# Optimization experiments

Measured on AMD Instinct MI355X. Metric: run time of the kernel, lower is better.

The kernel has to match this reference:

```python
import jax, jax.numpy as jnp
import numpy as np

B, G, D, H, DH, M, L, FF = 4, 16906, 256, 8, 32, 110, 6, 1024
EPS = 1e-4  # performer_pytorch softmax_kernel eps

def _ortho_proj(rng, m, d):
    # gaussian orthogonal random matrix (FAVOR+), rows scaled by chi norms
    blocks = []
    for _ in range(m // d):
        q, _ = np.linalg.qr(rng.standard_normal((d, d)))
        blocks.append(q.T)
    rem = m % d
    if rem:
        q, _ = np.linalg.qr(rng.standard_normal((d, d)))
        blocks.append(q.T[:rem])
    mat = np.concatenate(blocks, 0)
    mult = np.linalg.norm(rng.standard_normal((m, d)), axis=1)
    return (mult[:, None] * mat).astype(np.float32)

def setup_inputs():
    key = jax.random.key(0)
    ks = jax.random.split(key, 12)
    rng = np.random.default_rng(0)
    s = 0.02
    return {
        'expr': jax.random.uniform(ks[0], (B, G), jnp.float32),
        'token_emb': jax.random.normal(ks[1], (7, D)) * s,
        'cls_token': jax.random.normal(ks[2], (1, 1, D)),
        'ln1_g': jnp.ones((L, D)), 'ln1_b': jnp.zeros((L, D)),
        'wq': jax.random.normal(ks[3], (L, D, D)) * s, 'bq': jnp.zeros((L, D)),
        'wk': jax.random.normal(ks[4], (L, D, D)) * s, 'bk': jnp.zeros((L, D)),
        'wv': jax.random.normal(ks[5], (L, D, D)) * s, 'bv': jnp.zeros((L, D)),
        'wo': jax.random.normal(ks[6], (L, D, D)) * s, 'bo': jnp.zeros((L, D)),
        'ln2_g': jnp.ones((L, D)), 'ln2_b': jnp.zeros((L, D)),
        'w1': jax.random.normal(ks[7], (L, D, FF)) * s, 'b1': jnp.zeros((L, FF)),
        'w2': jax.random.normal(ks[8], (L, FF, D)) * s, 'b2': jnp.zeros((L, D)),
        'proj_w': jax.random.normal(ks[9], (D, D)) * s, 'proj_b': jnp.zeros((D,)),
        'projs': jnp.asarray(np.stack([_ortho_proj(rng, M, DH) for _ in range(L)])),
    }

def _ln(x, g, b):
    mu = jnp.mean(x, -1, keepdims=True)
    var = jnp.mean((x - mu) ** 2, -1, keepdims=True)
    return (x - mu) * jax.lax.rsqrt(var + 1e-5) * g + b

def _feat(x, proj, is_query):
    # FAVOR+ softmax kernel feature map. x: [b,h,n,dh], proj: [m,dh]
    xn = x * (DH ** -0.25)
    dd = jnp.einsum('bhnd,md->bhnm', xn, proj)
    diag = 0.5 * jnp.sum(xn * xn, -1, keepdims=True)
    stab = jnp.max(dd, -1, keepdims=True) if is_query else jnp.max(dd)
    return (M ** -0.5) * (jnp.exp(dd - diag - stab) + EPS)

def _heads(x, w, bias, b, n):
    return (x @ w + bias).reshape(b, n, H, DH).transpose(0, 2, 1, 3)

def _forward(expr, token_emb, cls_token, ln1_g, ln1_b, wq, bq, wk, bk, wv, bv,
             wo, bo, ln2_g, ln2_b, w1, b1, w2, b2, proj_w, proj_b, projs):
    b = expr.shape[0]
    # preprocess: L1-normalize, scale, log1p, 7-bin bucketize
    sexpr = expr / jnp.maximum(jnp.sum(jnp.abs(expr), -1, keepdims=True), 1e-12)
    e = jnp.log1p(sexpr * 1e4)
    bins = jnp.linspace(0.0, jnp.max(e), 8)[:7]
    tokens = jnp.clip(jnp.searchsorted(bins, e, side='left'), 0, 6)
    x = jnp.concatenate([jnp.broadcast_to(cls_token, (b, 1, D)), token_emb[tokens]], 1)
    n = x.shape[1]
    for l in range(L):
        h = _ln(x, ln1_g[l], ln1_b[l])
        q = _heads(h, wq[l], bq[l], b, n)
        k = _heads(h, wk[l], bk[l], b, n)
        v = _heads(h, wv[l], bv[l], b, n)
        qf = _feat(q, projs[l], True)
        kf = _feat(k, projs[l], False)
        # non-causal linear attention: phi(Q)(phi(K)^T V) / (phi(Q) sum phi(K))
        d_inv = 1.0 / jnp.einsum('bhnm,bhm->bhn', qf, jnp.sum(kf, 2))
        ctx = jnp.einsum('bhnm,bhnd->bhmd', kf, v)
        o = jnp.einsum('bhnm,bhmd,bhn->bhnd', qf, ctx, d_inv)
        x = x + o.transpose(0, 2, 1, 3).reshape(b, n, D) @ wo[l] + bo[l]
        h = _ln(x, ln2_g[l], ln2_b[l])
        x = x + jax.nn.gelu(h @ w1[l] + b1[l], approximate=False) @ w2[l] + b2[l]
    return x[:, 0] @ proj_w + proj_b

def reference(expr, token_emb, cls_token, ln1_g, ln1_b, wq, bq, wk, bk, wv, bv,
              wo, bo, ln2_g, ln2_b, w1, b1, w2, b2, proj_w, proj_b, projs):
    return _forward(expr, token_emb, cls_token, ln1_g, ln1_b, wq, bq, wk, bk, wv,
                    bv, wo, bo, ln2_g, ln2_b, w1, b1, w2, b2, proj_w, proj_b, projs)
```

## Files before the change

kernel.cpp:

```cpp
#include <hip/hip_runtime.h>
#include <math.h>

#define B_ 4
#define G_ 16906
#define D_ 256
#define H_ 8
#define DH_ 32
#define M_ 110
#define L_ 6
#define FF_ 1024
#define NSEQ (G_ + 1)
#define NR (B_ * NSEQ)
#define NRP_ 67712
#define NYT_ 529
#define BH_ 32
#define QS_ 768

static constexpr float SCALE_  = 0.42044820762685725f;
static constexpr float MSCALE_ = 0.09534625892455922f;
static constexpr float FEPS_   = 1e-4f;

#define SZP_ ((size_t)NRP_ * D_)
#define WS_FLOATS 92000000
__device__ float g_ws[WS_FLOATS];

typedef __attribute__((ext_vector_type(8))) short bh8;
typedef __attribute__((ext_vector_type(4))) float f4;

__device__ __forceinline__ unsigned f2u(float f){
    unsigned u = __float_as_uint(f);
    return (u & 0x80000000u) ? ~u : (u | 0x80000000u);
}
__device__ __forceinline__ float u2f(unsigned u){
    return (u & 0x80000000u) ? __uint_as_float(u & 0x7fffffffu) : __uint_as_float(~u);
}
__device__ __forceinline__ unsigned short f2b(float f){
    unsigned u = __float_as_uint(f);
    return (unsigned short)((u + 0x7fffu + ((u >> 16) & 1u)) >> 16);
}
__device__ __forceinline__ float bf2f(unsigned short u){
    return __uint_as_float(((unsigned)u) << 16);
}
__device__ __forceinline__ void gld16(const unsigned short* g, unsigned short* l){
    __builtin_amdgcn_global_load_lds((const __attribute__((address_space(1))) void*)g,
                                     (__attribute__((address_space(3))) void*)l, 16, 0, 0);
}

__global__ void k_pre_init(unsigned* __restrict__ maxkey){
    if (threadIdx.x == 0) *maxkey = 0x007fffffu;
}

__global__ void k_rowsum(const float* __restrict__ expr, float* __restrict__ ssum){
    int b = blockIdx.x, t = threadIdx.x;
    float s = 0.f;
    for (int g = t; g < G_; g += 256) s += fabsf(expr[(size_t)b * G_ + g]);
    __shared__ float red[256];
    red[t] = s; __syncthreads();
    for (int off = 128; off > 0; off >>= 1){ if (t < off) red[t] += red[t + off]; __syncthreads(); }
    if (t == 0) ssum[b] = red[0];
}

__global__ void k_compute_e(const float* __restrict__ expr, const float* __restrict__ ssum,
                            float* __restrict__ ebuf, unsigned* __restrict__ maxkey){
    int t = threadIdx.x;
    int idx = blockIdx.x * 256 + t;
    float e = -INFINITY;
    if (idx < B_ * G_){
        int b = idx / G_;
        float denom = fmaxf(ssum[b], 1e-12f);
        e = log1pf(expr[idx] / denom * 1e4f);
        ebuf[idx] = e;
    }
    __shared__ float red[256];
    red[t] = e; __syncthreads();
    for (int off = 128; off > 0; off >>= 1){ if (t < off) red[t] = fmaxf(red[t], red[t + off]); __syncthreads(); }
    if (t == 0) atomicMax(maxkey, f2u(red[0]));
}

__global__ void k_embed(const float* __restrict__ ebuf, const unsigned* __restrict__ maxkey,
                        const float* __restrict__ tokemb, const float* __restrict__ cls,
                        float* __restrict__ x){
    int row = blockIdx.x, t = threadIdx.x;
    if (row >= NR){ x[(size_t)row * D_ + t] = 0.f; return; }
    int b = row / NSEQ, i = row % NSEQ;
    float v;
    if (i == 0){
        v = cls[t];
    } else {
        float e = ebuf[(size_t)b * G_ + (i - 1)];
        float mx = u2f(*maxkey);
        float step = mx / 7.0f;
        int cnt = 0;
        #pragma unroll
        for (int j = 0; j < 7; ++j){
            float bin = step * (float)j;
            cnt += (bin < e) ? 1 : 0;
        }
        if (cnt > 6) cnt = 6;
        v = tokemb[cnt * D_ + t];
    }
    x[(size_t)row * D_ + t] = v;
}

__launch_bounds__(256)
__global__ void k_ln(const float* __restrict__ X, unsigned short* __restrict__ Y,
                     const float* __restrict__ g, const float* __restrict__ b){
    int wave = threadIdx.x >> 6, lane = threadIdx.x & 63;
    int row = blockIdx.x * 4 + wave;
    float4 v = *(const float4*)&X[(size_t)row * D_ + lane * 4];
    float s = v.x + v.y + v.z + v.w;
    s += __shfl_xor(s, 1);  s += __shfl_xor(s, 2);  s += __shfl_xor(s, 4);
    s += __shfl_xor(s, 8);  s += __shfl_xor(s, 16); s += __shfl_xor(s, 32);
    float mu = s * (1.0f / 256.0f);
    float d0 = v.x - mu, d1 = v.y - mu, d2 = v.z - mu, d3 = v.w - mu;
    float q = d0 * d0 + d1 * d1 + d2 * d2 + d3 * d3;
    q += __shfl_xor(q, 1);  q += __shfl_xor(q, 2);  q += __shfl_xor(q, 4);
    q += __shfl_xor(q, 8);  q += __shfl_xor(q, 16); q += __shfl_xor(q, 32);
    float inv = rsqrtf(q * (1.0f / 256.0f) + 1e-5f);
    float4 gv = *(const float4*)&g[lane * 4];
    float4 bv = *(const float4*)&b[lane * 4];
    ushort4 o;
    o.x = f2b(d0 * inv * gv.x + bv.x);
    o.y = f2b(d1 * inv * gv.y + bv.y);
    o.z = f2b(d2 * inv * gv.z + bv.z);
    o.w = f2b(d3 * inv * gv.w + bv.w);
    *(ushort4*)&Y[(size_t)row * D_ + lane * 4] = o;
}

__global__ void k_wconv(const float* __restrict__ Win, unsigned short* __restrict__ Wout,
                        int K, int N, int lstride){
    __shared__ float tile[32][33];
    int l = blockIdx.z;
    const float* W = Win + (size_t)l * K * N;
    unsigned short* O = Wout + (size_t)l * lstride;
    int n0 = blockIdx.x * 32, k0 = blockIdx.y * 32;
    int tx = threadIdx.x, ty = threadIdx.y;
    #pragma unroll
    for (int j = 0; j < 4; ++j)
        tile[ty + j * 8][tx] = W[(size_t)(k0 + ty + j * 8) * N + n0 + tx];
    __syncthreads();
    #pragma unroll
    for (int j = 0; j < 4; ++j){
        int n = ty + j * 8;
        O[(size_t)(n0 + n) * K + k0 + tx] = f2b(tile[tx][n]);
    }
}

__global__ void k_packbias(const float* __restrict__ bq, const float* __restrict__ bk,
                           const float* __restrict__ bv, float* __restrict__ o){
    int l = blockIdx.x, t = threadIdx.x;
    o[l * QS_ + t]        = bq[l * D_ + t];
    o[l * QS_ + 256 + t]  = bk[l * D_ + t];
    o[l * QS_ + 512 + t]  = bv[l * D_ + t];
}

#define ABUF_SH 4096
#define BUFS_SH 8192
#define EPIT 136
template <int MODE>
__launch_bounds__(256)
__global__ void gemm_bf16(const unsigned short* __restrict__ A,
                          const unsigned short* __restrict__ Wt,
                          const float* __restrict__ bias,
                          float* __restrict__ Cf, unsigned short* __restrict__ Cb,
                          int K, int N, int NY){
    int NX = N >> 7;
    int lid = blockIdx.x;
    int xcd = lid & 7, slot = lid >> 3;
    int colt = slot % NX;
    int rowt = (slot / NX) * 8 + xcd;
    if (rowt >= NY) return;
    int rowBase = rowt * 128, colBase = colt * 128;

    __shared__ __align__(16) unsigned short smem[2 * BUFS_SH];
    int tid = threadIdx.x;
    int lane = tid & 63, wave = tid >> 6;
    int wrow = (wave >> 1) * 64, wcol = (wave & 1) * 64;
    int m = lane & 15, kg = lane >> 4;

    int sr = tid >> 2, sc = tid & 3;
    int scs = sc ^ ((sr >> 1) & 3);
    const unsigned short* Ag = A  + (size_t)(rowBase + sr) * K + scs * 8;
    const unsigned short* Bg = Wt + (size_t)(colBase + sr) * K + scs * 8;
    int kc8 = (kg ^ ((m >> 1) & 3)) * 8;

    f4 acc[4][4];
    #pragma unroll
    for (int i = 0; i < 4; ++i)
        #pragma unroll
        for (int j = 0; j < 4; ++j) acc[i][j] = (f4){0.f, 0.f, 0.f, 0.f};

    auto stage = [&](int sel, int it){
        unsigned short* sb = smem + (sel ? BUFS_SH : 0);
        int k0 = it << 5;
        gld16(Ag + k0,                  sb + (tid << 3));
        gld16(Ag + (size_t)64 * K + k0, sb + 2048 + (tid << 3));
        gld16(Bg + k0,                  sb + ABUF_SH + (tid << 3));
        gld16(Bg + (size_t)64 * K + k0, sb + ABUF_SH + 2048 + (tid << 3));
    };

    stage(0, 0);
    const int NIT = K >> 5;
    for (int it = 0; it < NIT; ++it){
        int cur = (it & 1) ? BUFS_SH : 0;
        __syncthreads();
        if (it + 1 < NIT) stage((it + 1) & 1, it + 1);
        bh8 af[4], bf[4];
        #pragma unroll
        for (int mi = 0; mi < 4; ++mi)
            af[mi] = *(const bh8*)&smem[cur + (wrow + mi * 16 + m) * 32 + kc8];
        #pragma unroll
        for (int ni = 0; ni < 4; ++ni)
            bf[ni] = *(const bh8*)&smem[cur + ABUF_SH + (wcol + ni * 16 + m) * 32 + kc8];
        #pragma unroll
        for (int mi = 0; mi < 4; ++mi)
            #pragma unroll
            for (int ni = 0; ni < 4; ++ni)
                acc[mi][ni] = __builtin_amdgcn_mfma_f32_16x16x32_bf16(af[mi], bf[ni], acc[mi][ni], 0, 0, 0);
    }
    __syncthreads();
    int q4 = lane >> 4;
    if (MODE == 0 || MODE == 1){
        #pragma unroll
        for (int ni = 0; ni < 4; ++ni){
            int col = colBase + wcol + ni * 16 + m;
            float bv = bias[col];
            #pragma unroll
            for (int mi = 0; mi < 4; ++mi){
                int r0 = rowBase + wrow + mi * 16 + q4 * 4;
                #pragma unroll
                for (int rg = 0; rg < 4; ++rg){
                    int row = r0 + rg;
                    float v = acc[mi][ni][rg] + bv;
                    if (MODE == 1) v += Cf[(size_t)row * N + col];
                    Cf[(size_t)row * N + col] = v;
                }
            }
        }
    } else {
        #pragma unroll
        for (int half = 0; half < 2; ++half){
            if ((wrow >> 6) == half){
                #pragma unroll
                for (int ni = 0; ni < 4; ++ni){
                    int coll = wcol + ni * 16 + m;
                    float bv = bias[colBase + coll];
                    #pragma unroll
                    for (int mi = 0; mi < 4; ++mi){
                        int rl0 = (wrow & 63) + mi * 16 + q4 * 4;
                        #pragma unroll
                        for (int rg = 0; rg < 4; ++rg){
                            float v = acc[mi][ni][rg] + bv;
                            if (MODE == 2) v = 0.5f * v * (1.0f + erff(v * 0.70710678118654752f));
                            smem[(rl0 + rg) * EPIT + coll] = f2b(v);
                        }
                    }
                }
            }
            __syncthreads();
            #pragma unroll
            for (int p = 0; p < 4; ++p){
                int idx = p * 256 + tid;
                int r = idx >> 4, ch = idx & 15;
                int grow = rowBase + half * 64 + r;
                uint4 val = *(const uint4*)&smem[r * EPIT + ch * 8];
                *(uint4*)&Cb[(size_t)grow * N + colBase + ch * 8] = val;
            }
            __syncthreads();
        }
    }
}

__global__ void k_layer_init(float* __restrict__ kfsum, float* __restrict__ ctx,
                             unsigned* __restrict__ stab){
    int t = blockIdx.x * 256 + threadIdx.x;
    int nt = gridDim.x * 256;
    if (t == 0) *stab = 0x007fffffu;
    for (int i = t; i < BH_ * M_; i += nt) kfsum[i] = 0.f;
    for (int i = t; i < BH_ * M_ * DH_; i += nt) ctx[i] = 0.f;
}

__launch_bounds__(256)
__global__ void k_kmax(const unsigned short* __restrict__ qkv, const float* __restrict__ proj,
                       unsigned* __restrict__ stab, float* __restrict__ diagk){
    __shared__ __align__(16) unsigned short pjT[112 * 40];
    __shared__ __align__(16) unsigned short kl[32 * 40];
    __shared__ float red[256];
    int t = threadIdx.x, lane = t & 63, wave = t >> 6;
    int m16 = lane & 15, quad = lane >> 4;
    int bh = blockIdx.y, b = bh >> 3, hh = bh & 7;
    for (int e = t; e < 112 * 32; e += 256){
        int mm = e >> 5, d = e & 31;
        pjT[mm * 40 + d] = f2b((mm < M_) ? SCALE_ * proj[mm * DH_ + d] : 0.f);
    }
    int i0 = blockIdx.x * 256, i1 = min(i0 + 256, NSEQ);
    float mx = -INFINITY;
    int sr = t >> 2, sl = t & 3;
    __syncthreads();
    for (int t0 = i0; t0 < i1; t0 += 32){
        int rows = min(32, i1 - t0);
        if (t < 128){
            uint4 kv = (uint4){0,0,0,0};
            if (sr < rows)
                kv = *(const uint4*)(qkv + ((size_t)(b * NSEQ + t0 + sr)) * QS_ + 256 + hh * DH_ + sl * 8);
            *(uint4*)&kl[sr * 40 + sl * 8] = kv;
            const unsigned short* ks = (const unsigned short*)&kv;
            float ss = 0.f;
            #pragma unroll
            for (int j = 0; j < 8; ++j){ float xv = bf2f(ks[j]); ss += xv * xv; }
            ss += __shfl_xor(ss, 1); ss += __shfl_xor(ss, 2);
            if (sl == 0 && sr < rows)
                diagk[((size_t)(b * NSEQ + t0 + sr)) * 8 + hh] = 0.5f * SCALE_ * SCALE_ * ss;
        }
        __syncthreads();
        #pragma unroll
        for (int nn = 0; nn < 2; ++nn){
            int nt = wave + nn * 4;
            if (nt >= 7) continue;
            bh8 bfrag = *(const bh8*)&pjT[(nt * 16 + m16) * 40 + quad * 8];
            int f = nt * 16 + m16;
            #pragma unroll
            for (int mt = 0; mt < 2; ++mt){
                bh8 afrag = *(const bh8*)&kl[(mt * 16 + m16) * 40 + quad * 8];
                f4 dd = (f4){0.f,0.f,0.f,0.f};
                dd = __builtin_amdgcn_mfma_f32_16x16x32_bf16(afrag, bfrag, dd, 0, 0, 0);
                #pragma unroll
                for (int rg = 0; rg < 4; ++rg){
                    int r = mt * 16 + quad * 4 + rg;
                    if (f < M_ && r < rows) mx = fmaxf(mx, dd[rg]);
                }
            }
        }
        __syncthreads();
    }
    red[t] = mx; __syncthreads();
    for (int off = 128; off > 0; off >>= 1){ if (t < off) red[t] = fmaxf(red[t], red[t + off]); __syncthreads(); }
    if (t == 0) atomicMax(stab, f2u(red[0]));
}

__launch_bounds__(256)
__global__ void k_kv(const unsigned short* __restrict__ qkv,
                     const float* __restrict__ proj, const float* __restrict__ diagk,
                     const unsigned* __restrict__ stabkey,
                     float* __restrict__ kfsum, float* __restrict__ ctx){
    __shared__ __align__(16) unsigned short pjT[112 * 40];
    __shared__ __align__(16) unsigned short kl[32 * 40];
    __shared__ __align__(16) unsigned short vT[32 * 40];
    __shared__ __align__(16) unsigned short kfT[112 * 40];
    __shared__ float diagl[32];
    int t = threadIdx.x, lane = t & 63, wave = t >> 6;
    int m16 = lane & 15, quad = lane >> 4;
    int bh = blockIdx.y, b = bh >> 3, hh = bh & 7;
    for (int e = t; e < 112 * 32; e += 256){
        int mm = e >> 5, d = e & 31;
        pjT[mm * 40 + d] = f2b((mm < M_) ? SCALE_ * proj[mm * DH_ + d] : 0.f);
    }
    float stab = u2f(*stabkey);
    f4 acc[2][2];
    #pragma unroll
    for (int i = 0; i < 2; ++i)
        #pragma unroll
        for (int j = 0; j < 2; ++j) acc[i][j] = (f4){0.f,0.f,0.f,0.f};
    float ksum = 0.f;
    int i0 = blockIdx.x * 256, i1 = min(i0 + 256, NSEQ);
    int sr = t >> 2, sl = t & 3;
    __syncthreads();
    for (int t0 = i0; t0 < i1; t0 += 32){
        int rows = min(32, i1 - t0);
        if (t < 128){
            size_t base = ((size_t)(b * NSEQ + t0 + sr)) * QS_ + hh * DH_ + sl * 8;
            uint4 kv = (uint4){0,0,0,0}, vv = (uint4){0,0,0,0};
            if (sr < rows){
                kv = *(const uint4*)(qkv + base + 256);
                vv = *(const uint4*)(qkv + base + 512);
            }
            *(uint4*)&kl[sr * 40 + sl * 8] = kv;
            const unsigned short* vs = (const unsigned short*)&vv;
            #pragma unroll
            for (int j = 0; j < 8; ++j)
                vT[(sl * 8 + j) * 40 + sr] = vs[j];
        }
        if (t < 32) diagl[t] = (t < rows) ? diagk[((size_t)(b * NSEQ + t0 + t)) * 8 + hh] : 0.f;
        __syncthreads();
        #pragma unroll
        for (int nn = 0; nn < 2; ++nn){
            int nt = wave + nn * 4;
            if (nt >= 7) continue;
            bh8 bfrag = *(const bh8*)&pjT[(nt * 16 + m16) * 40 + quad * 8];
            int f = nt * 16 + m16;
            #pragma unroll
            for (int mt = 0; mt < 2; ++mt){
                bh8 afrag = *(const bh8*)&kl[(mt * 16 + m16) * 40 + quad * 8];
                f4 dd = (f4){0.f,0.f,0.f,0.f};
                dd = __builtin_amdgcn_mfma_f32_16x16x32_bf16(afrag, bfrag, dd, 0, 0, 0);
                #pragma unroll
                for (int rg = 0; rg < 4; ++rg){
                    int r = mt * 16 + quad * 4 + rg;
                    float kf = 0.f;
                    if (r < rows) kf = MSCALE_ * (__expf(dd[rg] - diagl[r] - stab) + FEPS_);
                    kfT[f * 40 + r] = f2b(kf);
                }
            }
        }
        __syncthreads();
        #pragma unroll
        for (int mm = 0; mm < 2; ++mm){
            int mt = wave + mm * 4;
            if (mt >= 7) continue;
            bh8 afrag = *(const bh8*)&kfT[(mt * 16 + m16) * 40 + quad * 8];
            #pragma unroll
            for (int nt2 = 0; nt2 < 2; ++nt2){
                bh8 bfrag = *(const bh8*)&vT[(nt2 * 16 + m16) * 40 + quad * 8];
                acc[mm][nt2] = __builtin_amdgcn_mfma_f32_16x16x32_bf16(afrag, bfrag, acc[mm][nt2], 0, 0, 0);
            }
        }
        if (t < M_){
            for (int i = 0; i < rows; ++i) ksum += bf2f(kfT[t * 40 + i]);
        }
        __syncthreads();
    }
    float* ctx_bh = ctx + (size_t)bh * M_ * DH_;
    #pragma unroll
    for (int mm = 0; mm < 2; ++mm){
        int mt = wave + mm * 4;
        if (mt >= 7) continue;
        #pragma unroll
        for (int nt2 = 0; nt2 < 2; ++nt2){
            #pragma unroll
            for (int rg = 0; rg < 4; ++rg){
                int f = mt * 16 + quad * 4 + rg;
                int dh = nt2 * 16 + m16;
                if (f < M_) atomicAdd(&ctx_bh[f * DH_ + dh], acc[mm][nt2][rg]);
            }
        }
    }
    if (t < M_) atomicAdd(&kfsum[bh * M_ + t], ksum);
}

#define CXP 136
__launch_bounds__(256)
__global__ void k_qattn(const unsigned short* __restrict__ qkv, const float* __restrict__ proj,
                        const float* __restrict__ kfsumg,
                        const float* __restrict__ ctxg, unsigned short* __restrict__ Ob){
    __shared__ __align__(16) unsigned short pjT[112 * 40];
    __shared__ __align__(16) unsigned short ql[32 * 40];
    __shared__ __align__(16) unsigned short qfl[32 * CXP];
    __shared__ __align__(16) unsigned short cxT[32 * CXP];
    __shared__ float kfs[112];
    __shared__ float diagl[32];
    __shared__ float rmax[4][32];
    __shared__ float denl[32];
    int t = threadIdx.x, lane = t & 63, wave = t >> 6;
    int m16 = lane & 15, quad = lane >> 4;
    int bh = blockIdx.y, b = bh >> 3, hh = bh & 7;
    const float* ctx_bh = ctxg + (size_t)bh * M_ * DH_;
    for (int e = t; e < 112 * 32; e += 256){
        int mm = e >> 5, d = e & 31;
        pjT[mm * 40 + d] = f2b((mm < M_) ? SCALE_ * proj[mm * DH_ + d] : 0.f);
    }
    for (int e = t; e < 32 * 128; e += 256){
        int dh = e >> 7, f = e & 127;
        cxT[dh * CXP + f] = f2b((f < M_) ? ctx_bh[f * DH_ + dh] : 0.f);
    }
    for (int e = t; e < 32 * CXP; e += 256) qfl[e] = 0;
    if (t < M_) kfs[t] = kfsumg[bh * M_ + t];
    int i0 = blockIdx.x * 256, i1 = min(i0 + 256, NSEQ);
    int sr = t >> 2, sl = t & 3;
    __syncthreads();
    for (int t0 = i0; t0 < i1; t0 += 32){
        int rows = min(32, i1 - t0);
        if (t < 128){
            uint4 qv = (uint4){0,0,0,0};
            if (sr < rows)
                qv = *(const uint4*)(qkv + ((size_t)(b * NSEQ + t0 + sr)) * QS_ + hh * DH_ + sl * 8);
            *(uint4*)&ql[sr * 40 + sl * 8] = qv;
        }
        __syncthreads();
        {
            int r = t >> 3, part = t & 7;
            float s = 0.f;
            #pragma unroll
            for (int d0 = 0; d0 < 4; ++d0){
                float qv2 = bf2f(ql[r * 40 + part * 4 + d0]);
                s += qv2 * qv2;
            }
            s += __shfl_xor(s, 1); s += __shfl_xor(s, 2); s += __shfl_xor(s, 4);
            if (part == 0) diagl[r] = 0.5f * SCALE_ * SCALE_ * s;
        }
        f4 ddv[2][2];
        float pm[2][4];
        #pragma unroll
        for (int mt = 0; mt < 2; ++mt)
            #pragma unroll
            for (int rg = 0; rg < 4; ++rg) pm[mt][rg] = -INFINITY;
        #pragma unroll
        for (int nn = 0; nn < 2; ++nn){
            int nt = wave + nn * 4;
            if (nt >= 7) continue;
            bh8 bfrag = *(const bh8*)&pjT[(nt * 16 + m16) * 40 + quad * 8];
            int f = nt * 16 + m16;
            #pragma unroll
            for (int mt = 0; mt < 2; ++mt){
                bh8 afrag = *(const bh8*)&ql[(mt * 16 + m16) * 40 + quad * 8];
                f4 dd = (f4){0.f,0.f,0.f,0.f};
                dd = __builtin_amdgcn_mfma_f32_16x16x32_bf16(afrag, bfrag, dd, 0, 0, 0);
                ddv[nn][mt] = dd;
                if (f < M_){
                    #pragma unroll
                    for (int rg = 0; rg < 4; ++rg) pm[mt][rg] = fmaxf(pm[mt][rg], dd[rg]);
                }
            }
        }
        #pragma unroll
        for (int mt = 0; mt < 2; ++mt)
            #pragma unroll
            for (int rg = 0; rg < 4; ++rg){
                float v = pm[mt][rg];
                v = fmaxf(v, __shfl_xor(v, 1));
                v = fmaxf(v, __shfl_xor(v, 2));
                v = fmaxf(v, __shfl_xor(v, 4));
                v = fmaxf(v, __shfl_xor(v, 8));
                if (m16 == 0) rmax[wave][mt * 16 + quad * 4 + rg] = v;
            }
        __syncthreads();
        #pragma unroll
        for (int nn = 0; nn < 2; ++nn){
            int nt = wave + nn * 4;
            if (nt >= 7) continue;
            int f = nt * 16 + m16;
            #pragma unroll
            for (int mt = 0; mt < 2; ++mt){
                #pragma unroll
                for (int rg = 0; rg < 4; ++rg){
                    int r = mt * 16 + quad * 4 + rg;
                    float mx = fmaxf(fmaxf(rmax[0][r], rmax[1][r]), fmaxf(rmax[2][r], rmax[3][r]));
                    float qf = MSCALE_ * (__expf(ddv[nn][mt][rg] - diagl[r] - mx) + FEPS_);
                    qfl[r * CXP + f] = f2b(qf);
                }
            }
        }
        __syncthreads();
        {
            int r = t >> 3, part = t & 7;
            float s = 0.f;
            for (int f = part; f < M_; f += 8) s += bf2f(qfl[r * CXP + f]) * kfs[f];
            s += __shfl_xor(s, 4); s += __shfl_xor(s, 2); s += __shfl_xor(s, 1);
            if (part == 0) denl[r] = s;
        }
        __syncthreads();
        {
            int mt = wave >> 1, nt = wave & 1;
            f4 oacc = (f4){0.f,0.f,0.f,0.f};
            #pragma unroll
            for (int kk = 0; kk < 4; ++kk){
                bh8 afrag = *(const bh8*)&qfl[(mt * 16 + m16) * CXP + kk * 32 + quad * 8];
                bh8 bfrag = *(const bh8*)&cxT[(nt * 16 + m16) * CXP + kk * 32 + quad * 8];
                oacc = __builtin_amdgcn_mfma_f32_16x16x32_bf16(afrag, bfrag, oacc, 0, 0, 0);
            }
            #pragma unroll
            for (int rg = 0; rg < 4; ++rg){
                int r = mt * 16 + quad * 4 + rg;
                if (r < rows){
                    int grow = b * NSEQ + t0 + r;
                    float o = oacc[rg] / denl[r];
                    Ob[(size_t)grow * D_ + hh * DH_ + nt * 16 + m16] = f2b(o);
                }
            }
        }
        __syncthreads();
    }
}

__global__ void k_final(const float* __restrict__ x, const float* __restrict__ pw,
                        const float* __restrict__ pb, float* __restrict__ out){
    int b = blockIdx.x, c = threadIdx.x;
    const float* xr = x + (size_t)b * NSEQ * D_;
    float s = pb[c];
    for (int k = 0; k < D_; ++k) s += xr[k] * pw[k * D_ + c];
    out[b * D_ + c] = s;
}

extern "C" void kernel_launch(void* const* d_in, const int* in_sizes, int n_in,
                              void* d_out, int out_size, void* d_ws, size_t ws_size,
                              hipStream_t stream){
    const float* expr   = (const float*)d_in[0];
    const float* tokemb = (const float*)d_in[1];
    const float* cls    = (const float*)d_in[2];
    const float* ln1g   = (const float*)d_in[3];
    const float* ln1b   = (const float*)d_in[4];
    const float* wq     = (const float*)d_in[5];
    const float* bq     = (const float*)d_in[6];
    const float* wk     = (const float*)d_in[7];
    const float* bk     = (const float*)d_in[8];
    const float* wv     = (const float*)d_in[9];
    const float* bv     = (const float*)d_in[10];
    const float* wo     = (const float*)d_in[11];
    const float* bo     = (const float*)d_in[12];
    const float* ln2g   = (const float*)d_in[13];
    const float* ln2b   = (const float*)d_in[14];
    const float* w1     = (const float*)d_in[15];
    const float* b1     = (const float*)d_in[16];
    const float* w2     = (const float*)d_in[17];
    const float* b2     = (const float*)d_in[18];
    const float* pw     = (const float*)d_in[19];
    const float* pb     = (const float*)d_in[20];
    const float* projs  = (const float*)d_in[21];
    float* out = (float*)d_out;

    float* ws = nullptr;
    if (ws_size >= WS_FLOATS * sizeof(float)) {
        ws = (float*)d_ws;
    } else {
        void* p = nullptr;
        hipGetSymbolAddress(&p, HIP_SYMBOL(g_ws));
        ws = (float*)p;
    }

    float* x = ws;
    unsigned short* hb = (unsigned short*)(x + SZP_);
    unsigned short* qkvb = hb + (size_t)NRP_ * D_;
    unsigned short* interb = qkvb + (size_t)NRP_ * QS_;
    unsigned short* wqkvT = interb + (size_t)NRP_ * FF_;
    unsigned short* woT = wqkvT + (size_t)L_ * QS_ * D_;
    unsigned short* w1T = woT + (size_t)L_ * D_ * D_;
    unsigned short* w2T = w1T + (size_t)L_ * D_ * FF_;
    float* bqkv  = (float*)(w2T + (size_t)L_ * FF_ * D_);
    float* diagk = bqkv + L_ * QS_ + 32;
    float* ebuf  = diagk + (size_t)NR * 8 + 32;
    float* ssum  = ebuf + B_ * G_;
    unsigned* maxkey = (unsigned*)(ssum + 8);
    unsigned* stab   = maxkey + 8;
    float* kfsum = (float*)(stab + 8);
    float* ctx   = kfsum + BH_ * M_ + 32;

    dim3 wb(32, 8);
    k_wconv<<<dim3(D_ / 32, D_ / 32, L_), wb, 0, stream>>>(wq, wqkvT,            D_, D_, QS_ * D_);
    k_wconv<<<dim3(D_ / 32, D_ / 32, L_), wb, 0, stream>>>(wk, wqkvT + 256 * D_, D_, D_, QS_ * D_);
    k_wconv<<<dim3(D_ / 32, D_ / 32, L_), wb, 0, stream>>>(wv, wqkvT + 512 * D_, D_, D_, QS_ * D_);
    k_wconv<<<dim3(D_ / 32, D_ / 32, L_), wb, 0, stream>>>(wo, woT, D_, D_, D_ * D_);
    k_wconv<<<dim3(FF_ / 32, D_ / 32, L_), wb, 0, stream>>>(w1, w1T, D_, FF_, D_ * FF_);
    k_wconv<<<dim3(D_ / 32, FF_ / 32, L_), wb, 0, stream>>>(w2, w2T, FF_, D_, FF_ * D_);
    k_packbias<<<L_, 256, 0, stream>>>(bq, bk, bv, bqkv);

    k_pre_init<<<1, 64, 0, stream>>>(maxkey);
    k_rowsum<<<B_, 256, 0, stream>>>(expr, ssum);
    k_compute_e<<<(B_ * G_ + 255) / 256, 256, 0, stream>>>(expr, ssum, ebuf, maxkey);
    k_embed<<<NRP_, 256, 0, stream>>>(ebuf, maxkey, tokemb, cls, x);

    const int NYC = (NYT_ + 7) / 8;
    int gQKV = 8 * NYC * (QS_ / 128);
    int gWO  = 8 * NYC * (D_ / 128);
    int gF1  = 8 * NYC * (FF_ / 128);
    int gF2  = 8 * NYC * (D_ / 128);
    dim3 gBH((NSEQ + 255) / 256, 32);
    int gLN = NRP_ / 4;

    for (int l = 0; l < L_; ++l){
        const float* pjl = projs + (size_t)l * M_ * DH_;
        k_ln<<<gLN, 256, 0, stream>>>(x, hb, ln1g + l * D_, ln1b + l * D_);
        gemm_bf16<3><<<gQKV, 256, 0, stream>>>(hb, wqkvT + (size_t)l * QS_ * D_, bqkv + l * QS_,
                                               nullptr, qkvb, D_, QS_, NYT_);
        k_layer_init<<<64, 256, 0, stream>>>(kfsum, ctx, stab);
        k_kmax<<<gBH, 256, 0, stream>>>(qkvb, pjl, stab, diagk);
        k_kv<<<gBH, 256, 0, stream>>>(qkvb, pjl, diagk, stab, kfsum, ctx);
        k_qattn<<<gBH, 256, 0, stream>>>(qkvb, pjl, kfsum, ctx, hb);
        gemm_bf16<1><<<gWO, 256, 0, stream>>>(hb, woT + (size_t)l * D_ * D_, bo + l * D_,
                                              x, nullptr, D_, D_, NYT_);
        k_ln<<<gLN, 256, 0, stream>>>(x, hb, ln2g + l * D_, ln2b + l * D_);
        gemm_bf16<2><<<gF1, 256, 0, stream>>>(hb, w1T + (size_t)l * D_ * FF_, b1 + l * FF_,
                                              nullptr, interb, D_, FF_, NYT_);
        gemm_bf16<1><<<gF2, 256, 0, stream>>>(interb, w2T + (size_t)l * FF_ * D_, b2 + l * D_,
                                              x, nullptr, FF_, D_, NYT_);
    }
    k_final<<<B_, 256, 0, stream>>>(x, pw, pb, out);
}
```

Measured before the change: 3.750 ms.

## Restructure FAVOR attention kernels to per-wave row tiles without block barriers

The k_kmax, k_kv and k_qattn kernels now give each wave its own 32-row tile. Each wave loads K/Q MFMA fragments straight from global memory and keeps all 7 feature tiles in registers, instead of staging through shared memory with __syncthreads between phases. The diagonal term is recomputed in-wave with shuffles, which removes the diagk global buffer. k_kv reduces through shared-memory atomics before the global atomics, and k_qattn does the row max and denominator with wave shuffles. This trades higher register pressure and unaligned row loads for fewer barriers and less global traffic.

```diff
diff --git a/kernel.cpp b/kernel.cpp
--- a/kernel.cpp
+++ b/kernel.cpp
@@ -280,11 +280,11 @@
     for (int i = t; i < BH_ * M_ * DH_; i += nt) ctx[i] = 0.f;
 }
 
+
 __launch_bounds__(256)
 __global__ void k_kmax(const unsigned short* __restrict__ qkv, const float* __restrict__ proj,
-                       unsigned* __restrict__ stab, float* __restrict__ diagk){
+                       unsigned* __restrict__ stab){
     __shared__ __align__(16) unsigned short pjT[112 * 40];
-    __shared__ __align__(16) unsigned short kl[32 * 40];
     __shared__ float red[256];
     int t = threadIdx.x, lane = t & 63, wave = t >> 6;
     int m16 = lane & 15, quad = lane >> 4;
@@ -293,45 +293,33 @@
         int mm = e >> 5, d = e & 31;
         pjT[mm * 40 + d] = f2b((mm < M_) ? SCALE_ * proj[mm * DH_ + d] : 0.f);
     }
+    __syncthreads();
+    bh8 pj[7];
+    #pragma unroll
+    for (int nt = 0; nt < 7; ++nt)
+        pj[nt] = *(const bh8*)&pjT[(nt * 16 + m16) * 40 + quad * 8];
     int i0 = blockIdx.x * 256, i1 = min(i0 + 256, NSEQ);
     float mx = -INFINITY;
-    int sr = t >> 2, sl = t & 3;
-    __syncthreads();
-    for (int t0 = i0; t0 < i1; t0 += 32){
+    for (int t0 = i0 + wave * 32; t0 < i1; t0 += 128){
         int rows = min(32, i1 - t0);
-        if (t < 128){
-            uint4 kv = (uint4){0,0,0,0};
-            if (sr < rows)
-                kv = *(const uint4*)(qkv + ((size_t)(b * NSEQ + t0 + sr)) * QS_ + 256 + hh * DH_ + sl * 8);
-            *(uint4*)&kl[sr * 40 + sl * 8] = kv;
-            const unsigned short* ks = (const unsigned short*)&kv;
-            float ss = 0.f;
-            #pragma unroll
-            for (int j = 0; j < 8; ++j){ float xv = bf2f(ks[j]); ss += xv * xv; }
-            ss += __shfl_xor(ss, 1); ss += __shfl_xor(ss, 2);
-            if (sl == 0 && sr < rows)
-                diagk[((size_t)(b * NSEQ + t0 + sr)) * 8 + hh] = 0.5f * SCALE_ * SCALE_ * ss;
-        }
-        __syncthreads();
-        #pragma unroll
-        for (int nn = 0; nn < 2; ++nn){
-            int nt = wave + nn * 4;
-            if (nt >= 7) continue;
-            bh8 bfrag = *(const bh8*)&pjT[(nt * 16 + m16) * 40 + quad * 8];
+        size_t rb = (size_t)(b * NSEQ + t0);
+        bh8 a0 = *(const bh8*)(qkv + (rb + m16) * QS_ + 256 + hh * DH_ + quad * 8);
+        bh8 a1 = *(const bh8*)(qkv + (rb + 16 + m16) * QS_ + 256 + hh * DH_ + quad * 8);
+        #pragma unroll
+        for (int nt = 0; nt < 7; ++nt){
             int f = nt * 16 + m16;
-            #pragma unroll
-            for (int mt = 0; mt < 2; ++mt){
-                bh8 afrag = *(const bh8*)&kl[(mt * 16 + m16) * 40 + quad * 8];
-                f4 dd = (f4){0.f,0.f,0.f,0.f};
-                dd = __builtin_amdgcn_mfma_f32_16x16x32_bf16(afrag, bfrag, dd, 0, 0, 0);
+            f4 d0 = (f4){0.f,0.f,0.f,0.f}, d1 = (f4){0.f,0.f,0.f,0.f};
+            d0 = __builtin_amdgcn_mfma_f32_16x16x32_bf16(a0, pj[nt], d0, 0, 0, 0);
+            d1 = __builtin_amdgcn_mfma_f32_16x16x32_bf16(a1, pj[nt], d1, 0, 0, 0);
+            if (f < M_){
                 #pragma unroll
                 for (int rg = 0; rg < 4; ++rg){
-                    int r = mt * 16 + quad * 4 + rg;
-                    if (f < M_ && r < rows) mx = fmaxf(mx, dd[rg]);
+                    int r0 = quad * 4 + rg;
+                    if (r0 < rows)      mx = fmaxf(mx, d0[rg]);
+                    if (r0 + 16 < rows) mx = fmaxf(mx, d1[rg]);
                 }
             }
         }
-        __syncthreads();
     }
     red[t] = mx; __syncthreads();
     for (int off = 128; off > 0; off >>= 1){ if (t < off) red[t] = fmaxf(red[t], red[t + off]); __syncthreads(); }
@@ -340,14 +328,14 @@
 
 __launch_bounds__(256)
 __global__ void k_kv(const unsigned short* __restrict__ qkv,
-                     const float* __restrict__ proj, const float* __restrict__ diagk,
+                     const float* __restrict__ proj,
                      const unsigned* __restrict__ stabkey,
                      float* __restrict__ kfsum, float* __restrict__ ctx){
     __shared__ __align__(16) unsigned short pjT[112 * 40];
-    __shared__ __align__(16) unsigned short kl[32 * 40];
-    __shared__ __align__(16) unsigned short vT[32 * 40];
-    __shared__ __align__(16) unsigned short kfT[112 * 40];
-    __shared__ float diagl[32];
+    __shared__ __align__(16) unsigned short vT[4][32 * 40];
+    __shared__ __align__(16) unsigned short kfs[4][16 * 40];
+    __shared__ float ctx_l[M_ * DH_];
+    __shared__ float ksum_l[112];
     int t = threadIdx.x, lane = t & 63, wave = t >> 6;
     int m16 = lane & 15, quad = lane >> 4;
     int bh = blockIdx.y, b = bh >> 3, hh = bh & 7;
@@ -355,86 +343,104 @@
         int mm = e >> 5, d = e & 31;
         pjT[mm * 40 + d] = f2b((mm < M_) ? SCALE_ * proj[mm * DH_ + d] : 0.f);
     }
+    for (int e = t; e < M_ * DH_; e += 256) ctx_l[e] = 0.f;
+    if (t < 112) ksum_l[t] = 0.f;
+    __syncthreads();
     float stab = u2f(*stabkey);
-    f4 acc[2][2];
-    #pragma unroll
-    for (int i = 0; i < 2; ++i)
-        #pragma unroll
-        for (int j = 0; j < 2; ++j) acc[i][j] = (f4){0.f,0.f,0.f,0.f};
-    float ksum = 0.f;
+    unsigned short* vTw = &vT[wave][0];
+    unsigned short* kfw = &kfs[wave][0];
+    f4 acc[7][2];
+    #pragma unroll
+    for (int i = 0; i < 7; ++i){ acc[i][0] = (f4){0.f,0.f,0.f,0.f}; acc[i][1] = (f4){0.f,0.f,0.f,0.f}; }
+    float ksr[7];
+    #pragma unroll
+    for (int i = 0; i < 7; ++i) ksr[i] = 0.f;
     int i0 = blockIdx.x * 256, i1 = min(i0 + 256, NSEQ);
-    int sr = t >> 2, sl = t & 3;
+    int vr = lane & 31, vc = lane >> 5;
+    for (int t0 = i0 + wave * 32; t0 < i1; t0 += 128){
+        int rows = min(32, i1 - t0);
+        size_t rb = (size_t)(b * NSEQ + t0);
+        bh8 a0 = *(const bh8*)(qkv + (rb + m16) * QS_ + 256 + hh * DH_ + quad * 8);
+        bh8 a1 = *(const bh8*)(qkv + (rb + 16 + m16) * QS_ + 256 + hh * DH_ + quad * 8);
+        float s0 = 0.f, s1 = 0.f;
+        {
+            const unsigned short* p0 = (const unsigned short*)&a0;
+            const unsigned short* p1 = (const unsigned short*)&a1;
+            #pragma unroll
+            for (int j = 0; j < 8; ++j){
+                float x0 = bf2f(p0[j]); s0 += x0 * x0;
+                float x1 = bf2f(p1[j]); s1 += x1 * x1;
+            }
+            s0 += __shfl_xor(s0, 16); s0 += __shfl_xor(s0, 32);
+            s1 += __shfl_xor(s1, 16); s1 += __shfl_xor(s1, 32);
+            s0 *= 0.5f * SCALE_ * SCALE_;
+            s1 *= 0.5f * SCALE_ * SCALE_;
+        }
+        {
+            uint4 v0 = (uint4){0,0,0,0}, v1 = (uint4){0,0,0,0};
+            if (vr < rows){
+                const unsigned short* vrow = qkv + (rb + vr) * QS_ + 512 + hh * DH_;
+                v0 = *(const uint4*)(vrow + vc * 16);
+                v1 = *(const uint4*)(vrow + vc * 16 + 8);
+            }
+            const unsigned short* q0 = (const unsigned short*)&v0;
+            const unsigned short* q1 = (const unsigned short*)&v1;
+            #pragma unroll
+            for (int j = 0; j < 8; ++j){
+                vTw[(vc * 16 + j) * 40 + vr]     = q0[j];
+                vTw[(vc * 16 + 8 + j) * 40 + vr] = q1[j];
+            }
+        }
+        #pragma unroll
+        for (int nt = 0; nt < 7; ++nt){
+            bh8 pjf = *(const bh8*)&pjT[(nt * 16 + m16) * 40 + quad * 8];
+            f4 d0 = (f4){0.f,0.f,0.f,0.f}, d1 = (f4){0.f,0.f,0.f,0.f};
+            d0 = __builtin_amdgcn_mfma_f32_16x16x32_bf16(a0, pjf, d0, 0, 0, 0);
+            d1 = __builtin_amdgcn_mfma_f32_16x16x32_bf16(a1, pjf, d1, 0, 0, 0);
+            int f = nt * 16 + m16;
+            float kacc = 0.f;
+            #pragma unroll
+            for (int rg = 0; rg < 4; ++rg){
+                int r0 = quad * 4 + rg;
+                float dg0 = __shfl(s0, r0);
+                float dg1 = __shfl(s1, r0);
+                float k0 = 0.f, k1 = 0.f;
+                if (f < M_){
+                    if (r0 < rows)      k0 = MSCALE_ * (__expf(d0[rg] - dg0 - stab) + FEPS_);
+                    if (r0 + 16 < rows) k1 = MSCALE_ * (__expf(d1[rg] - dg1 - stab) + FEPS_);
+                }
+                kacc += k0 + k1;
+                kfw[m16 * 40 + r0]      = f2b(k0);
+                kfw[m16 * 40 + 16 + r0] = f2b(k1);
+            }
+            ksr[nt] += kacc;
+            bh8 kaf = *(const bh8*)&kfw[m16 * 40 + quad * 8];
+            bh8 vb0 = *(const bh8*)&vTw[m16 * 40 + quad * 8];
+            bh8 vb1 = *(const bh8*)&vTw[(16 + m16) * 40 + quad * 8];
+            acc[nt][0] = __builtin_amdgcn_mfma_f32_16x16x32_bf16(kaf, vb0, acc[nt][0], 0, 0, 0);
+            acc[nt][1] = __builtin_amdgcn_mfma_f32_16x16x32_bf16(kaf, vb1, acc[nt][1], 0, 0, 0);
+        }
+    }
+    #pragma unroll
+    for (int nt = 0; nt < 7; ++nt){
+        float ks = ksr[nt];
+        ks += __shfl_xor(ks, 16); ks += __shfl_xor(ks, 32);
+        int f = nt * 16 + m16;
+        if (quad == 0 && f < M_) atomicAdd(&ksum_l[f], ks);
+    }
+    #pragma unroll
+    for (int nt = 0; nt < 7; ++nt)
+        #pragma unroll
+        for (int dt = 0; dt < 2; ++dt)
+            #pragma unroll
+            for (int rg = 0; rg < 4; ++rg){
+                int f = nt * 16 + quad * 4 + rg;
+                if (f < M_) atomicAdd(&ctx_l[f * DH_ + dt * 16 + m16], acc[nt][dt][rg]);
+            }
     __syncthreads();
-    for (int t0 = i0; t0 < i1; t0 += 32){
-        int rows = min(32, i1 - t0);
-        if (t < 128){
-            size_t base = ((size_t)(b * NSEQ + t0 + sr)) * QS_ + hh * DH_ + sl * 8;
-            uint4 kv = (uint4){0,0,0,0}, vv = (uint4){0,0,0,0};
-            if (sr < rows){
-                kv = *(const uint4*)(qkv + base + 256);
-                vv = *(const uint4*)(qkv + base + 512);
-            }
-            *(uint4*)&kl[sr * 40 + sl * 8] = kv;
-            const unsigned short* vs = (const unsigned short*)&vv;
-            #pragma unroll
-            for (int j = 0; j < 8; ++j)
-                vT[(sl * 8 + j) * 40 + sr] = vs[j];
-        }
-        if (t < 32) diagl[t] = (t < rows) ? diagk[((size_t)(b * NSEQ + t0 + t)) * 8 + hh] : 0.f;
-        __syncthreads();
-        #pragma unroll
-        for (int nn = 0; nn < 2; ++nn){
-            int nt = wave + nn * 4;
-            if (nt >= 7) continue;
-            bh8 bfrag = *(const bh8*)&pjT[(nt * 16 + m16) * 40 + quad * 8];
-            int f = nt * 16 + m16;
-            #pragma unroll
-            for (int mt = 0; mt < 2; ++mt){
-                bh8 afrag = *(const bh8*)&kl[(mt * 16 + m16) * 40 + quad * 8];
-                f4 dd = (f4){0.f,0.f,0.f,0.f};
-                dd = __builtin_amdgcn_mfma_f32_16x16x32_bf16(afrag, bfrag, dd, 0, 0, 0);
-                #pragma unroll
-                for (int rg = 0; rg < 4; ++rg){
-                    int r = mt * 16 + quad * 4 + rg;
-                    float kf = 0.f;
-                    if (r < rows) kf = MSCALE_ * (__expf(dd[rg] - diagl[r] - stab) + FEPS_);
-                    kfT[f * 40 + r] = f2b(kf);
-                }
-            }
-        }
-        __syncthreads();
-        #pragma unroll
-        for (int mm = 0; mm < 2; ++mm){
-            int mt = wave + mm * 4;
-            if (mt >= 7) continue;
-            bh8 afrag = *(const bh8*)&kfT[(mt * 16 + m16) * 40 + quad * 8];
-            #pragma unroll
-            for (int nt2 = 0; nt2 < 2; ++nt2){
-                bh8 bfrag = *(const bh8*)&vT[(nt2 * 16 + m16) * 40 + quad * 8];
-                acc[mm][nt2] = __builtin_amdgcn_mfma_f32_16x16x32_bf16(afrag, bfrag, acc[mm][nt2], 0, 0, 0);
-            }
-        }
-        if (t < M_){
-            for (int i = 0; i < rows; ++i) ksum += bf2f(kfT[t * 40 + i]);
-        }
-        __syncthreads();
-    }
     float* ctx_bh = ctx + (size_t)bh * M_ * DH_;
-    #pragma unroll
-    for (int mm = 0; mm < 2; ++mm){
-        int mt = wave + mm * 4;
-        if (mt >= 7) continue;
-        #pragma unroll
-        for (int nt2 = 0; nt2 < 2; ++nt2){
-            #pragma unroll
-            for (int rg = 0; rg < 4; ++rg){
-                int f = mt * 16 + quad * 4 + rg;
-                int dh = nt2 * 16 + m16;
-                if (f < M_) atomicAdd(&ctx_bh[f * DH_ + dh], acc[mm][nt2][rg]);
-            }
-        }
-    }
-    if (t < M_) atomicAdd(&kfsum[bh * M_ + t], ksum);
+    for (int e = t; e < M_ * DH_; e += 256) atomicAdd(&ctx_bh[e], ctx_l[e]);
+    if (t < M_) atomicAdd(&kfsum[bh * M_ + t], ksum_l[t]);
 }
 
 #define CXP 136
@@ -443,13 +449,8 @@
                         const float* __restrict__ kfsumg,
                         const float* __restrict__ ctxg, unsigned short* __restrict__ Ob){
     __shared__ __align__(16) unsigned short pjT[112 * 40];
-    __shared__ __align__(16) unsigned short ql[32 * 40];
-    __shared__ __align__(16) unsigned short qfl[32 * CXP];
     __shared__ __align__(16) unsigned short cxT[32 * CXP];
-    __shared__ float kfs[112];
-    __shared__ float diagl[32];
-    __shared__ float rmax[4][32];
-    __shared__ float denl[32];
+    __shared__ __align__(16) unsigned short qfs[4][32 * CXP];
     int t = threadIdx.x, lane = t & 63, wave = t >> 6;
     int m16 = lane & 15, quad = lane >> 4;
     int bh = blockIdx.y, b = bh >> 3, hh = bh & 7;
@@ -462,112 +463,135 @@
         int dh = e >> 7, f = e & 127;
         cxT[dh * CXP + f] = f2b((f < M_) ? ctx_bh[f * DH_ + dh] : 0.f);
     }
-    for (int e = t; e < 32 * CXP; e += 256) qfl[e] = 0;
-    if (t < M_) kfs[t] = kfsumg[bh * M_ + t];
+    {
+        unsigned short* qw = &qfs[wave][0];
+        int r = lane & 31, c0 = 112 + (lane >> 5) * 8;
+        #pragma unroll
+        for (int j = 0; j < 8; ++j) qw[r * CXP + c0 + j] = 0;
+    }
+    __syncthreads();
+    float kfsr[7];
+    #pragma unroll
+    for (int nt = 0; nt < 7; ++nt){
+        int f = nt * 16 + m16;
+        kfsr[nt] = (f < M_) ? kfsumg[bh * M_ + f] : 0.f;
+    }
+    bh8 cxf[2][4];
+    #pragma unroll
+    for (int dt = 0; dt < 2; ++dt)
+        #pragma unroll
+        for (int kk = 0; kk < 4; ++kk)
+            cxf[dt][kk] = *(const bh8*)&cxT[(dt * 16 + m16) * CXP + kk * 32 + quad * 8];
+    unsigned short* qw = &qfs[wave][0];
     int i0 = blockIdx.x * 256, i1 = min(i0 + 256, NSEQ);
-    int sr = t >> 2, sl = t & 3;
-    __syncthreads();
-    for (int t0 = i0; t0 < i1; t0 += 32){
+    for (int t0 = i0 + wave * 32; t0 < i1; t0 += 128){
         int rows = min(32, i1 - t0);
-        if (t < 128){
-            uint4 qv = (uint4){0,0,0,0};
-            if (sr < rows)
-                qv = *(const uint4*)(qkv + ((size_t)(b * NSEQ + t0 + sr)) * QS_ + hh * DH_ + sl * 8);
-            *(uint4*)&ql[sr * 40 + sl * 8] = qv;
-        }
-        __syncthreads();
+        size_t rb = (size_t)(b * NSEQ + t0);
+        bh8 a0 = *(const bh8*)(qkv + (rb + m16) * QS_ + hh * DH_ + quad * 8);
+        bh8 a1 = *(const bh8*)(qkv + (rb + 16 + m16) * QS_ + hh * DH_ + quad * 8);
+        float s0 = 0.f, s1 = 0.f;
         {
-            int r = t >> 3, part = t & 7;
-            float s = 0.f;
-            #pragma unroll
-            for (int d0 = 0; d0 < 4; ++d0){
-                float qv2 = bf2f(ql[r * 40 + part * 4 + d0]);
-                s += qv2 * qv2;
-            }
-            s += __shfl_xor(s, 1); s += __shfl_xor(s, 2); s += __shfl_xor(s, 4);
-            if (part == 0) diagl[r] = 0.5f * SCALE_ * SCALE_ * s;
-        }
-        f4 ddv[2][2];
-        float pm[2][4];
-        #pragma unroll
-        for (int mt = 0; mt < 2; ++mt)
-            #pragma unroll
-            for (int rg = 0; rg < 4; ++rg) pm[mt][rg] = -INFINITY;
-        #pragma unroll
-        for (int nn = 0; nn < 2; ++nn){
-            int nt = wave + nn * 4;
-            if (nt >= 7) continue;
-            bh8 bfrag = *(const bh8*)&pjT[(nt * 16 + m16) * 40 + quad * 8];
-            int f = nt * 16 + m16;
-            #pragma unroll
-            for (int mt = 0; mt < 2; ++mt){
-                bh8 afrag = *(const bh8*)&ql[(mt * 16 + m16) * 40 + quad * 8];
-                f4 dd = (f4){0.f,0.f,0.f,0.f};
-                dd = __builtin_amdgcn_mfma_f32_16x16x32_bf16(afrag, bfrag, dd, 0, 0, 0);
-                ddv[nn][mt] = dd;
-                if (f < M_){
-                    #pragma unroll
-                    for (int rg = 0; rg < 4; ++rg) pm[mt][rg] = fmaxf(pm[mt][rg], dd[rg]);
-                }
-            }
-        }
-        #pragma unroll
-        for (int mt = 0; mt < 2; ++mt)
-            #pragma unroll
-            for (int rg = 0; rg < 4; ++rg){
-                float v = pm[mt][rg];
-                v = fmaxf(v, __shfl_xor(v, 1));
-                v = fmaxf(v, __shfl_xor(v, 2));
-                v = fmaxf(v, __shfl_xor(v, 4));
-                v = fmaxf(v, __shfl_xor(v, 8));
-                if (m16 == 0) rmax[wave][mt * 16 + quad * 4 + rg] = v;
-            }
-        __syncthreads();
-        #pragma unroll
-        for (int nn = 0; nn < 2; ++nn){
-            int nt = wave + nn * 4;
-            if (nt >= 7) continue;
-            int f = nt * 16 + m16;
-            #pragma unroll
-            for (int mt = 0; mt < 2; ++mt){
+            const unsigned short* p0 = (const unsigned short*)&a0;
+            const unsigned short* p1 = (const unsigned short*)&a1;
+            #pragma unroll
+            for (int j = 0; j < 8; ++j){
+                float x0 = bf2f(p0[j]); s0 += x0 * x0;
+                float x1 = bf2f(p1[j]); s1 += x1 * x1;
+            }
+            s0 += __shfl_xor(s0, 16); s0 += __shfl_xor(s0, 32);
+            s1 += __shfl_xor(s1, 16); s1 += __shfl_xor(s1, 32);
+            s0 *= 0.5f * SCALE_ * SCALE_;
+            s1 *= 0.5f * SCALE_ * SCALE_;
+        }
+        f4 dv0[7], dv1[7];
+        #pragma unroll
+        for (int nt = 0; nt < 7; ++nt){
+            bh8 pjf = *(const bh8*)&pjT[(nt * 16 + m16) * 40 + quad * 8];
+            f4 d0 = (f4){0.f,0.f,0.f,0.f}, d1 = (f4){0.f,0.f,0.f,0.f};
+            dv0[nt] = __builtin_amdgcn_mfma_f32_16x16x32_bf16(a0, pjf, d0, 0, 0, 0);
+            dv1[nt] = __builtin_amdgcn_mfma_f32_16x16x32_bf16(a1, pjf, d1, 0, 0, 0);
+        }
+        float rm0[4], rm1[4];
+        #pragma unroll
+        for (int rg = 0; rg < 4; ++rg){ rm0[rg] = -INFINITY; rm1[rg] = -INFINITY; }
+        #pragma unroll
+        for (int nt = 0; nt < 7; ++nt){
+            if (nt * 16 + m16 < M_){
                 #pragma unroll
                 for (int rg = 0; rg < 4; ++rg){
-                    int r = mt * 16 + quad * 4 + rg;
-                    float mx = fmaxf(fmaxf(rmax[0][r], rmax[1][r]), fmaxf(rmax[2][r], rmax[3][r]));
-                    float qf = MSCALE_ * (__expf(ddv[nn][mt][rg] - diagl[r] - mx) + FEPS_);
-                    qfl[r * CXP + f] = f2b(qf);
+                    rm0[rg] = fmaxf(rm0[rg], dv0[nt][rg]);
+                    rm1[rg] = fmaxf(rm1[rg], dv1[nt][rg]);
                 }
             }
         }
-        __syncthreads();
-        {
-            int r = t >> 3, part = t & 7;
-            float s = 0.f;
-            for (int f = part; f < M_; f += 8) s += bf2f(qfl[r * CXP + f]) * kfs[f];
-            s += __shfl_xor(s, 4); s += __shfl_xor(s, 2); s += __shfl_xor(s, 1);
-            if (part == 0) denl[r] = s;
-        }
-        __syncthreads();
-        {
-            int mt = wave >> 1, nt = wave & 1;
-            f4 oacc = (f4){0.f,0.f,0.f,0.f};
-            #pragma unroll
-            for (int kk = 0; kk < 4; ++kk){
-                bh8 afrag = *(const bh8*)&qfl[(mt * 16 + m16) * CXP + kk * 32 + quad * 8];
-                bh8 bfrag = *(const bh8*)&cxT[(nt * 16 + m16) * CXP + kk * 32 + quad * 8];
-                oacc = __builtin_amdgcn_mfma_f32_16x16x32_bf16(afrag, bfrag, oacc, 0, 0, 0);
-            }
+        #pragma unroll
+        for (int rg = 0; rg < 4; ++rg){
+            float v = rm0[rg];
+            v = fmaxf(v, __shfl_xor(v, 1)); v = fmaxf(v, __shfl_xor(v, 2));
+            v = fmaxf(v, __shfl_xor(v, 4)); v = fmaxf(v, __shfl_xor(v, 8));
+            rm0[rg] = v;
+            v = rm1[rg];
+            v = fmaxf(v, __shfl_xor(v, 1)); v = fmaxf(v, __shfl_xor(v, 2));
+            v = fmaxf(v, __shfl_xor(v, 4)); v = fmaxf(v, __shfl_xor(v, 8));
+            rm1[rg] = v;
+        }
+        float dg0[4], dg1[4];
+        #pragma unroll
+        for (int rg = 0; rg < 4; ++rg){
+            dg0[rg] = __shfl(s0, quad * 4 + rg);
+            dg1[rg] = __shfl(s1, quad * 4 + rg);
+        }
+        float den0[4], den1[4];
+        #pragma unroll
+        for (int rg = 0; rg < 4; ++rg){ den0[rg] = 0.f; den1[rg] = 0.f; }
+        #pragma unroll
+        for (int nt = 0; nt < 7; ++nt){
+            int f = nt * 16 + m16;
             #pragma unroll
             for (int rg = 0; rg < 4; ++rg){
-                int r = mt * 16 + quad * 4 + rg;
-                if (r < rows){
-                    int grow = b * NSEQ + t0 + r;
-                    float o = oacc[rg] / denl[r];
-                    Ob[(size_t)grow * D_ + hh * DH_ + nt * 16 + m16] = f2b(o);
+                int r0 = quad * 4 + rg;
+                float q0 = 0.f, q1 = 0.f;
+                if (f < M_){
+                    q0 = MSCALE_ * (__expf(dv0[nt][rg] - dg0[rg] - rm0[rg]) + FEPS_);
+                    q1 = MSCALE_ * (__expf(dv1[nt][rg] - dg1[rg] - rm1[rg]) + FEPS_);
                 }
-            }
-        }
-        __syncthreads();
+                qw[r0 * CXP + f]        = f2b(q0);
+                qw[(16 + r0) * CXP + f] = f2b(q1);
+                den0[rg] += q0 * kfsr[nt];
+                den1[rg] += q1 * kfsr[nt];
+            }
+        }
+        #pragma unroll
+        for (int rg = 0; rg < 4; ++rg){
+            float v = den0[rg];
+            v += __shfl_xor(v, 1); v += __shfl_xor(v, 2);
+            v += __shfl_xor(v, 4); v += __shfl_xor(v, 8);
+            den0[rg] = v;
+            v = den1[rg];
+            v += __shfl_xor(v, 1); v += __shfl_xor(v, 2);
+            v += __shfl_xor(v, 4); v += __shfl_xor(v, 8);
+            den1[rg] = v;
+        }
+        #pragma unroll
+        for (int rt = 0; rt < 2; ++rt){
+            #pragma unroll
+            for (int dt = 0; dt < 2; ++dt){
+                f4 o = (f4){0.f,0.f,0.f,0.f};
+                #pragma unroll
+                for (int kk = 0; kk < 4; ++kk){
+                    bh8 qa = *(const bh8*)&qw[(rt * 16 + m16) * CXP + kk * 32 + quad * 8];
+                    o = __builtin_amdgcn_mfma_f32_16x16x32_bf16(qa, cxf[dt][kk], o, 0, 0, 0);
+                }
+                #pragma unroll
+                for (int rg = 0; rg < 4; ++rg){
+                    int r = rt * 16 + quad * 4 + rg;
+                    if (r < rows){
+                        float den = rt ? den1[rg] : den0[rg];
+                        Ob[(rb + r) * D_ + hh * DH_ + dt * 16 + m16] = f2b(o[rg] / den);
+                    }
+                }
+            }
+        }
     }
 }
 
@@ -661,8 +685,8 @@
         gemm_bf16<3><<<gQKV, 256, 0, stream>>>(hb, wqkvT + (size_t)l * QS_ * D_, bqkv + l * QS_,
                                                nullptr, qkvb, D_, QS_, NYT_);
         k_layer_init<<<64, 256, 0, stream>>>(kfsum, ctx, stab);
-        k_kmax<<<gBH, 256, 0, stream>>>(qkvb, pjl, stab, diagk);
-        k_kv<<<gBH, 256, 0, stream>>>(qkvb, pjl, diagk, stab, kfsum, ctx);
+        k_kmax<<<gBH, 256, 0, stream>>>(qkvb, pjl, stab);
+        k_kv<<<gBH, 256, 0, stream>>>(qkvb, pjl, stab, kfsum, ctx);
         k_qattn<<<gBH, 256, 0, stream>>>(qkvb, pjl, kfsum, ctx, hb);
         gemm_bf16<1><<<gWO, 256, 0, stream>>>(hb, woT + (size_t)l * D_ * D_, bo + l * D_,
                                               x, nullptr, D_, D_, NYT_);
```

Measured after the change: 4.269 ms. 13.8% more time.
